# Performance work log

Measured on AMD Instinct MI355X. Metric: run time of the kernel, lower is better.

The kernel has to match this reference:

```python
import jax, jax.numpy as jnp
import numpy as np

N = 50000
NEG_SLOPE_ATT = 0.2    # PyG GATConv attention leaky_relu slope
NEG_SLOPE_ACT = 0.01   # torch F.leaky_relu default slope


def leaky(x, s):
    return jnp.where(x >= 0, x, s * x)


def gat_conv(x, src, dst, W, att_src, att_dst, bias):
    """PyG GATConv (concat=True, dropout off, self-loops already in src/dst).
    x: [N, F_in]; W: [F_in, H*C]; att_src/att_dst: [H, C]; bias: [H*C]."""
    H, C = att_src.shape
    h = (x @ W).reshape(N, H, C)                       # [N, H, C]
    a_src = (h * att_src[None]).sum(-1)                # [N, H]
    a_dst = (h * att_dst[None]).sum(-1)                # [N, H]
    e = leaky(a_src[src] + a_dst[dst], NEG_SLOPE_ATT)  # [E, H]
    # numerically-stable softmax over incoming edges of each dst node
    m = jax.ops.segment_max(e, dst, num_segments=N)    # [N, H]
    ex = jnp.exp(e - m[dst])
    Z = jax.ops.segment_sum(ex, dst, num_segments=N)   # [N, H]
    alpha = ex / (Z[dst] + 1e-16)                      # [E, H]
    msg = h[src] * alpha[:, :, None]                   # [E, H, C]
    out = jax.ops.segment_sum(msg, dst, num_segments=N)
    return out.reshape(N, H * C) + bias[None, :]


def setup_inputs() -> dict:
    key = jax.random.key(0)
    ks = jax.random.split(key, 12)
    E = 800000
    in_c, hid, heads, out_c = 256, 32, 4, 128
    hc = hid * heads  # 128
    x = jax.random.normal(ks[0], (N, in_c), dtype=jnp.float32)
    edge_index = jax.random.randint(ks[1], (2, E), 0, N, dtype=jnp.int64)
    s1 = 1.0 / np.sqrt(in_c)
    s2 = 1.0 / np.sqrt(hc)
    return {
        "x": x,
        "edge_index": edge_index,
        "W1": jax.random.normal(ks[2], (in_c, heads * hid), dtype=jnp.float32) * s1,
        "att_src1": jax.random.normal(ks[3], (heads, hid), dtype=jnp.float32) * s2,
        "att_dst1": jax.random.normal(ks[4], (heads, hid), dtype=jnp.float32) * s2,
        "b1": jnp.zeros((hc,), dtype=jnp.float32),
        "W2": jax.random.normal(ks[5], (hc, out_c), dtype=jnp.float32) * s2,
        "att_src2": jax.random.normal(ks[6], (1, out_c), dtype=jnp.float32) * s2,
        "att_dst2": jax.random.normal(ks[7], (1, out_c), dtype=jnp.float32) * s2,
        "b2": jnp.zeros((out_c,), dtype=jnp.float32),
    }


def reference(x, edge_index, W1, att_src1, att_dst1, b1, W2, att_src2, att_dst2, b2):
    # add self loops (PyG GATConv default add_self_loops=True)
    loops = jnp.arange(N, dtype=edge_index.dtype)
    src = jnp.concatenate([edge_index[0], loops])
    dst = jnp.concatenate([edge_index[1], loops])
    h = leaky(gat_conv(x, src, dst, W1, att_src1, att_dst1, b1), NEG_SLOPE_ACT)
    out = leaky(gat_conv(h, src, dst, W2, att_src2, att_dst2, b2), NEG_SLOPE_ACT)
    return out
```

## Files before the change

kernel.cpp:

```cpp
#include <hip/hip_runtime.h>
#include <hip/hip_fp16.h>

#define SLOPE_ATT 0.2f
#define SLOPE_ACT 0.01f

#define NB_CSR 128
#define CHUNK 8192

typedef _Float16 hf8 __attribute__((ext_vector_type(8)));
typedef float f32x4 __attribute__((ext_vector_type(4)));

template<int K, int H, bool A_FP32>
__device__ __forceinline__
void gemm_mfma_body(int gbid, int tid,
                    const void* __restrict__ Av, const _Float16* __restrict__ BT,
                    const float* __restrict__ att_s, const float* __restrict__ att_d,
                    _Float16* __restrict__ hout, float* __restrict__ a_src,
                    float* __restrict__ a_dst, int M)
{
  const int lane = tid & 63;
  const int wid  = tid >> 6;
  const int li   = lane & 15;
  const int lk   = lane >> 4;
  const int rowbase = gbid * 128 + wid * 32;

  const float*    Af = (const float*)Av;
  const _Float16* Ah = (const _Float16*)Av;

  f32x4 acc[2][8];
#pragma unroll
  for (int i = 0; i < 2; ++i)
#pragma unroll
    for (int j = 0; j < 8; ++j) acc[i][j] = (f32x4){0.f, 0.f, 0.f, 0.f};

  const int r0 = min(rowbase + li,      M - 1);
  const int r1 = min(rowbase + 16 + li, M - 1);

#pragma unroll
  for (int ks = 0; ks < K / 32; ++ks) {
    const int kb = ks * 32 + lk * 8;
    hf8 a0, a1;
    if constexpr (A_FP32) {
      const float* p0 = &Af[(size_t)r0 * K + kb];
      const float* p1 = &Af[(size_t)r1 * K + kb];
      float4 x0a = *(const float4*)p0, x0b = *(const float4*)(p0 + 4);
      float4 x1a = *(const float4*)p1, x1b = *(const float4*)(p1 + 4);
      a0[0]=(_Float16)x0a.x; a0[1]=(_Float16)x0a.y; a0[2]=(_Float16)x0a.z; a0[3]=(_Float16)x0a.w;
      a0[4]=(_Float16)x0b.x; a0[5]=(_Float16)x0b.y; a0[6]=(_Float16)x0b.z; a0[7]=(_Float16)x0b.w;
      a1[0]=(_Float16)x1a.x; a1[1]=(_Float16)x1a.y; a1[2]=(_Float16)x1a.z; a1[3]=(_Float16)x1a.w;
      a1[4]=(_Float16)x1b.x; a1[5]=(_Float16)x1b.y; a1[6]=(_Float16)x1b.z; a1[7]=(_Float16)x1b.w;
    } else {
      a0 = *(const hf8*)&Ah[(size_t)r0 * K + kb];
      a1 = *(const hf8*)&Ah[(size_t)r1 * K + kb];
    }
#pragma unroll
    for (int cf = 0; cf < 8; ++cf) {
      hf8 b = *(const hf8*)&BT[(size_t)(cf * 16 + li) * K + kb];
      acc[0][cf] = __builtin_amdgcn_mfma_f32_16x16x32_f16(a0, b, acc[0][cf], 0, 0, 0);
      acc[1][cf] = __builtin_amdgcn_mfma_f32_16x16x32_f16(a1, b, acc[1][cf], 0, 0, 0);
    }
  }

  float sA[8], dA[8];
#pragma unroll
  for (int cf = 0; cf < 8; ++cf) {
    sA[cf] = att_s[cf * 16 + li];
    dA[cf] = att_d[cf * 16 + li];
  }

  const bool full = (rowbase + 32) <= M;
#pragma unroll
  for (int rf = 0; rf < 2; ++rf) {
    const int rb = rowbase + rf * 16 + lk * 4;
#pragma unroll
    for (int reg = 0; reg < 4; ++reg) {
      const int r = rb + reg;
      if (full || r < M) {
#pragma unroll
        for (int cf = 0; cf < 8; ++cf)
          hout[(size_t)r * 128 + cf * 16 + li] = (_Float16)acc[rf][cf][reg];
      }
    }
    if constexpr (H == 4) {
#pragma unroll
      for (int hh = 0; hh < 4; ++hh) {
#pragma unroll
        for (int reg = 0; reg < 4; ++reg) {
          float sp = acc[rf][2*hh][reg] * sA[2*hh] + acc[rf][2*hh+1][reg] * sA[2*hh+1];
          float dp = acc[rf][2*hh][reg] * dA[2*hh] + acc[rf][2*hh+1][reg] * dA[2*hh+1];
          sp += __shfl_xor(sp, 1); sp += __shfl_xor(sp, 2);
          sp += __shfl_xor(sp, 4); sp += __shfl_xor(sp, 8);
          dp += __shfl_xor(dp, 1); dp += __shfl_xor(dp, 2);
          dp += __shfl_xor(dp, 4); dp += __shfl_xor(dp, 8);
          const int r = rb + reg;
          if (li == 0 && r < M) {
            a_src[(size_t)r * 4 + hh] = sp;
            a_dst[(size_t)r * 4 + hh] = dp;
          }
        }
      }
    } else {
#pragma unroll
      for (int reg = 0; reg < 4; ++reg) {
        float sp = 0.f, dp = 0.f;
#pragma unroll
        for (int cf = 0; cf < 8; ++cf) {
          sp += acc[rf][cf][reg] * sA[cf];
          dp += acc[rf][cf][reg] * dA[cf];
        }
        sp += __shfl_xor(sp, 1); sp += __shfl_xor(sp, 2);
        sp += __shfl_xor(sp, 4); sp += __shfl_xor(sp, 8);
        dp += __shfl_xor(dp, 1); dp += __shfl_xor(dp, 2);
        dp += __shfl_xor(dp, 4); dp += __shfl_xor(dp, 8);
        const int r = rb + reg;
        if (li == 0 && r < M) { a_src[r] = sp; a_dst[r] = dp; }
      }
    }
  }
}

template<int K, int H, bool A_FP32>
__global__ __launch_bounds__(256)
void gemm_mfma_kernel(const void* __restrict__ Av, const _Float16* __restrict__ BT,
                      const float* __restrict__ att_s, const float* __restrict__ att_d,
                      _Float16* __restrict__ hout, float* __restrict__ a_src,
                      float* __restrict__ a_dst, int M)
{
  gemm_mfma_body<K, H, A_FP32>(blockIdx.x, threadIdx.x, Av, BT, att_s, att_d,
                               hout, a_src, a_dst, M);
}

__global__ __launch_bounds__(256)
void fused_pre_kernel(const int* __restrict__ ei, int E, int N,
                      unsigned short* __restrict__ cnt16mat,
                      unsigned short* __restrict__ rank16,
                      const float* __restrict__ W1, _Float16* __restrict__ W1T,
                      const float* __restrict__ W2, _Float16* __restrict__ W2T,
                      int ncount)
{
  __shared__ unsigned cnt[CHUNK];
  const int bid = blockIdx.x;
  if (bid < ncount) {
    const int b = bid % NB_CSR;
    const int c0 = (bid / NB_CSR) * CHUNK;
    const int clen = min(CHUNK, N - c0);
    const int EE = E + N;
    const int epb = (EE + NB_CSR - 1) / NB_CSR;
    const int lo = b * epb, hi = min(lo + epb, EE);

    for (int j = threadIdx.x; j < clen; j += 256) cnt[j] = 0;
    __syncthreads();
    for (int i = lo + threadIdx.x; i < hi; i += 256) {
      int d = (i < E) ? ei[E + i] : (i - E);
      int r = d - c0;
      if (r >= 0 && r < clen) {
        unsigned rank = atomicAdd(&cnt[r], 1u);
        rank16[i] = (unsigned short)rank;
      }
    }
    __syncthreads();
    for (int j = threadIdx.x; j < clen; j += 256)
      cnt16mat[(size_t)b * N + c0 + j] = (unsigned short)cnt[j];
  } else {
    int rem = bid - ncount;
    if (rem < 128) {
      int idx = rem * 256 + threadIdx.x;
      int k = idx >> 7, c = idx & 127;
      W1T[(size_t)c * 256 + k] = (_Float16)W1[idx];
    } else {
      int idx = (rem - 128) * 256 + threadIdx.x;
      int k = idx >> 7, c = idx & 127;
      W2T[(size_t)c * 128 + k] = (_Float16)W2[idx];
    }
  }
}

__global__ __launch_bounds__(256)
void colscan_kernel(unsigned short* __restrict__ cnt16mat,
                    unsigned* __restrict__ deg, unsigned* __restrict__ bsum, int N)
{
  __shared__ unsigned red[256];
  const int d2 = blockIdx.x * 256 + threadIdx.x;
  const int N2 = N >> 1;
  unsigned off0 = 0, off1 = 0;
  if (d2 < N2) {
    unsigned* pm = (unsigned*)cnt16mat;
#pragma unroll 8
    for (int b = 0; b < NB_CSR; ++b) {
      unsigned t = pm[(size_t)b * N2 + d2];
      pm[(size_t)b * N2 + d2] = off0 | (off1 << 16);
      off0 += t & 0xFFFFu;
      off1 += t >> 16;
    }
    deg[2 * d2]     = off0;
    deg[2 * d2 + 1] = off1;
  }
  red[threadIdx.x] = off0 + off1;
  __syncthreads();
  for (int o = 128; o; o >>= 1) {
    if (threadIdx.x < o) red[threadIdx.x] += red[threadIdx.x + o];
    __syncthreads();
  }
  if (threadIdx.x == 0) bsum[blockIdx.x] = red[0];
}

__global__ __launch_bounds__(256)
void rowstart_kernel(const unsigned* __restrict__ deg, const unsigned* __restrict__ bsum,
                     unsigned* __restrict__ row_start, int N, int nblk)
{
  __shared__ unsigned s[256];
  __shared__ unsigned boff_sh;
  const int t = threadIdx.x;
  unsigned v0 = (t < nblk) ? bsum[t] : 0u;
  s[t] = v0;
  __syncthreads();
  for (int off = 1; off < 256; off <<= 1) {
    unsigned v = (t >= off) ? s[t - off] : 0u;
    __syncthreads();
    s[t] += v;
    __syncthreads();
  }
  if (t == (int)blockIdx.x) boff_sh = s[t] - v0;
  __syncthreads();
  const unsigned boff = boff_sh;
  __syncthreads();
  const int i = blockIdx.x * 512 + t * 2;
  unsigned d0 = (i < N) ? deg[i] : 0u;
  unsigned d1 = (i + 1 < N) ? deg[i + 1] : 0u;
  s[t] = d0 + d1;
  __syncthreads();
  for (int off = 1; off < 256; off <<= 1) {
    unsigned v = (t >= off) ? s[t - off] : 0u;
    __syncthreads();
    s[t] += v;
    __syncthreads();
  }
  unsigned base = boff + s[t] - (d0 + d1);
  if (i < N)     row_start[i] = base;
  if (i + 1 < N) row_start[i + 1] = base + d0;
}

__global__ __launch_bounds__(256)
void fused_mid_kernel(const int* __restrict__ ei, int E, int N, int epb,
                      const unsigned short* __restrict__ cnt16mat,
                      const unsigned short* __restrict__ rank16,
                      const unsigned* __restrict__ row_start,
                      unsigned* __restrict__ csr_src,
                      const float* __restrict__ x, const _Float16* __restrict__ W1T,
                      const float* __restrict__ as1, const float* __restrict__ ad1,
                      _Float16* __restrict__ h, float* __restrict__ asv,
                      float* __restrict__ adv, int ggrid)
{
  const int bid = blockIdx.x;
  if (bid < ggrid) {
    gemm_mfma_body<256, 4, true>(bid, threadIdx.x, x, W1T, as1, ad1,
                                 h, asv, adv, N);
  } else {
    const int i = (bid - ggrid) * 256 + threadIdx.x;
    const int EE = E + N;
    if (i < EE) {
      int s, d;
      if (i < E) { s = ei[i]; d = ei[E + i]; } else { s = d = i - E; }
      const int b = i / epb;
      unsigned pos = row_start[d] + cnt16mat[(size_t)b * N + d] + rank16[i];
      csr_src[pos] = (unsigned)s;
    }
  }
}

template<int H, bool OUT_HALF>
__global__ __launch_bounds__(256)
void aggregate_kernel(const unsigned* __restrict__ row_start,
                      const unsigned* __restrict__ deg,
                      const unsigned* __restrict__ csr_src,
                      const __half* __restrict__ h,
                      const float* __restrict__ a_src,
                      const float* __restrict__ a_dst,
                      const float* __restrict__ bias,
                      void* __restrict__ outv, int N)
{
  const int lane = threadIdx.x & 63;
  const int wid  = threadIdx.x >> 6;
  const int l5   = lane & 15;
  const int n    = blockIdx.x * 16 + wid * 4 + (lane >> 4);
  const int nn   = min(n, N - 1);
  const int hd   = (H == 4) ? (l5 >> 2) : 0;

  const float adn = a_dst[(size_t)nn * H + hd];
  const unsigned beg = row_start[nn];
  const unsigned cnt = deg[nn];
  unsigned cmax = cnt;
  cmax = max(cmax, (unsigned)__shfl_xor((int)cmax, 16));
  cmax = max(cmax, (unsigned)__shfl_xor((int)cmax, 32));

  const float4* __restrict__ h4 = (const float4*)h;

  float Z = 0.f;
  float acc[8];
#pragma unroll
  for (int j = 0; j < 8; ++j) acc[j] = 0.f;

  unsigned i = 0;
  for (; i + 2 <= cmax; i += 2) {
    unsigned s0 = csr_src[beg + min(i,     cnt - 1)];
    unsigned s1 = csr_src[beg + min(i + 1, cnt - 1)];
    float e0 = a_src[(size_t)s0 * H + hd] + adn;
    float e1 = a_src[(size_t)s1 * H + hd] + adn;
    float4 v0 = h4[(size_t)s0 * 16 + l5];
    float4 v1 = h4[(size_t)s1 * 16 + l5];
    e0 = (e0 >= 0.f) ? e0 : SLOPE_ATT * e0;
    e1 = (e1 >= 0.f) ? e1 : SLOPE_ATT * e1;
    float w0 = (i     < cnt) ? __expf(e0) : 0.f;
    float w1 = (i + 1 < cnt) ? __expf(e1) : 0.f;
    Z += w0 + w1;
    const __half2* p0 = (const __half2*)&v0;
    const __half2* p1 = (const __half2*)&v1;
#pragma unroll
    for (int j = 0; j < 4; ++j) {
      float2 f0 = __half22float2(p0[j]);
      float2 f1 = __half22float2(p1[j]);
      acc[2*j]   += w0 * f0.x + w1 * f1.x;
      acc[2*j+1] += w0 * f0.y + w1 * f1.y;
    }
  }
  if (i < cmax) {
    unsigned s0 = csr_src[beg + min(i, cnt - 1)];
    float e0 = a_src[(size_t)s0 * H + hd] + adn;
    float4 v0 = h4[(size_t)s0 * 16 + l5];
    e0 = (e0 >= 0.f) ? e0 : SLOPE_ATT * e0;
    float w0 = (i < cnt) ? __expf(e0) : 0.f;
    Z += w0;
    const __half2* p0 = (const __half2*)&v0;
#pragma unroll
    for (int j = 0; j < 4; ++j) {
      float2 f0 = __half22float2(p0[j]);
      acc[2*j]   += w0 * f0.x;
      acc[2*j+1] += w0 * f0.y;
    }
  }

  const float inv = 1.f / (Z + 1e-16f);
  float4 b0 = ((const float4*)bias)[l5 * 2];
  float4 b1 = ((const float4*)bias)[l5 * 2 + 1];
  float o[8];
  o[0] = acc[0] * inv + b0.x;  o[1] = acc[1] * inv + b0.y;
  o[2] = acc[2] * inv + b0.z;  o[3] = acc[3] * inv + b0.w;
  o[4] = acc[4] * inv + b1.x;  o[5] = acc[5] * inv + b1.y;
  o[6] = acc[6] * inv + b1.z;  o[7] = acc[7] * inv + b1.w;
#pragma unroll
  for (int j = 0; j < 8; ++j) o[j] = (o[j] >= 0.f) ? o[j] : SLOPE_ACT * o[j];

  if (n < N) {
    if constexpr (OUT_HALF) {
      union { __half2 q[4]; float4 f; } u;
      u.q[0] = __floats2half2_rn(o[0], o[1]);
      u.q[1] = __floats2half2_rn(o[2], o[3]);
      u.q[2] = __floats2half2_rn(o[4], o[5]);
      u.q[3] = __floats2half2_rn(o[6], o[7]);
      ((float4*)outv)[(size_t)n * 16 + l5] = u.f;
    } else {
      ((float4*)outv)[(size_t)n * 32 + l5 * 2]     = make_float4(o[0], o[1], o[2], o[3]);
      ((float4*)outv)[(size_t)n * 32 + l5 * 2 + 1] = make_float4(o[4], o[5], o[6], o[7]);
    }
  }
}

extern "C" void kernel_launch(void* const* d_in, const int* in_sizes, int n_in,
                              void* d_out, int out_size, void* d_ws, size_t ws_size,
                              hipStream_t stream)
{
  const float* x   = (const float*)d_in[0];
  const int*   ei  = (const int*)d_in[1];
  const float* W1  = (const float*)d_in[2];
  const float* as1 = (const float*)d_in[3];
  const float* ad1 = (const float*)d_in[4];
  const float* b1  = (const float*)d_in[5];
  const float* W2  = (const float*)d_in[6];
  const float* as2 = (const float*)d_in[7];
  const float* ad2 = (const float*)d_in[8];
  const float* b2  = (const float*)d_in[9];
  float* out = (float*)d_out;

  const int N  = in_sizes[0] / 256;
  const int E  = in_sizes[1] / 2;
  const int EE = E + N;
  const int NCH  = (N + CHUNK - 1) / CHUNK;
  const int nblk = (N + 511) / 512;
  const int NSC  = NB_CSR * NCH;
  const int epb  = (EE + NB_CSR - 1) / NB_CSR;

  float* ws = (float*)d_ws;
  size_t o = 0;
  _Float16* h    = (_Float16*)(ws + o); o += (size_t)N * 64;
  _Float16* act1 = (_Float16*)(ws + o); o += (size_t)N * 64;
  float* asv = ws + o; o += (size_t)N * 4;
  float* adv = ws + o; o += (size_t)N * 4;
  _Float16* W1T = (_Float16*)(ws + o); o += 128 * 256 / 2;
  _Float16* W2T = (_Float16*)(ws + o); o += 128 * 128 / 2;
  unsigned* deg       = (unsigned*)(ws + o); o += (size_t)N;
  unsigned* row_start = (unsigned*)(ws + o); o += (size_t)N;
  unsigned* bsum      = (unsigned*)(ws + o); o += 256;
  unsigned* csr_src   = (unsigned*)(ws + o); o += (size_t)EE;
  unsigned short* cnt16mat = (unsigned short*)(ws + o); o += (size_t)NB_CSR * N / 2;
  unsigned short* rank16   = (unsigned short*)(ws + o); o += (size_t)(EE + 1) / 2;

  const int ngrid = (N + 15) / 16;
  const int ggrid = (N + 127) / 128;
  const int sgrid = (EE + 255) / 256;

  fused_pre_kernel<<<NSC + 128 + 64, 256, 0, stream>>>(
      ei, E, N, cnt16mat, rank16, W1, W1T, W2, W2T, NSC);
  colscan_kernel<<<nblk, 256, 0, stream>>>(cnt16mat, deg, bsum, N);
  rowstart_kernel<<<nblk, 256, 0, stream>>>(deg, bsum, row_start, N, nblk);
  fused_mid_kernel<<<ggrid + sgrid, 256, 0, stream>>>(
      ei, E, N, epb, cnt16mat, rank16, row_start, csr_src,
      x, W1T, as1, ad1, h, asv, adv, ggrid);
  aggregate_kernel<4, true><<<ngrid, 256, 0, stream>>>(
      row_start, deg, csr_src, (const __half*)h, asv, adv, b1, act1, N);
  gemm_mfma_kernel<128, 1, false><<<ggrid, 256, 0, stream>>>(
      act1, W2T, as2, ad2, h, asv, adv, N);
  aggregate_kernel<1, false><<<ngrid, 256, 0, stream>>>(
      row_start, deg, csr_src, (const __half*)h, asv, adv, b2, out, N);
}
```

Baseline: 175.5 us.

## Fuse layer-1 aggregation with layer-2 GEMM and attention dots via LDS

The layer-1 aggregate kernel now writes each 16-node activation tile into shared memory and runs the layer-2 128x128 projection in the same block with MFMA. It also computes the layer-2 attention dot products using LDS atomics. This removes the act1 round trip through global memory and one kernel launch. In exchange the aggregation kernel gains LDS use, two block barriers and per-block W2T loads from global/L2, and uses small 16-row GEMM tiles that reuse weights less than the old 128-row GEMM did.

```diff
diff --git a/kernel.cpp b/kernel.cpp
--- a/kernel.cpp
+++ b/kernel.cpp
@@ -119,17 +119,6 @@
   }
 }
 
-template<int K, int H, bool A_FP32>
-__global__ __launch_bounds__(256)
-void gemm_mfma_kernel(const void* __restrict__ Av, const _Float16* __restrict__ BT,
-                      const float* __restrict__ att_s, const float* __restrict__ att_d,
-                      _Float16* __restrict__ hout, float* __restrict__ a_src,
-                      float* __restrict__ a_dst, int M)
-{
-  gemm_mfma_body<K, H, A_FP32>(blockIdx.x, threadIdx.x, Av, BT, att_s, att_d,
-                               hout, a_src, a_dst, M);
-}
-
 __global__ __launch_bounds__(256)
 void fused_pre_kernel(const int* __restrict__ ei, int E, int N,
                       unsigned short* __restrict__ cnt16mat,
@@ -268,25 +257,32 @@
   }
 }
 
-template<int H, bool OUT_HALF>
 __global__ __launch_bounds__(256)
-void aggregate_kernel(const unsigned* __restrict__ row_start,
-                      const unsigned* __restrict__ deg,
-                      const unsigned* __restrict__ csr_src,
-                      const __half* __restrict__ h,
-                      const float* __restrict__ a_src,
-                      const float* __restrict__ a_dst,
-                      const float* __restrict__ bias,
-                      void* __restrict__ outv, int N)
-{
+void agg1_gemm2_kernel(const unsigned* __restrict__ row_start,
+                       const unsigned* __restrict__ deg,
+                       const unsigned* __restrict__ csr_src,
+                       const __half* __restrict__ h,
+                       const float* __restrict__ a_src,
+                       const float* __restrict__ a_dst,
+                       const float* __restrict__ bias,
+                       const _Float16* __restrict__ W2T,
+                       const float* __restrict__ as2, const float* __restrict__ ad2,
+                       _Float16* __restrict__ h2,
+                       float* __restrict__ asv2, float* __restrict__ adv2, int N)
+{
+  __shared__ _Float16 actS[16][136];
+  __shared__ float sdots[2][16];
+
   const int lane = threadIdx.x & 63;
   const int wid  = threadIdx.x >> 6;
   const int l5   = lane & 15;
-  const int n    = blockIdx.x * 16 + wid * 4 + (lane >> 4);
+  const int nl   = wid * 4 + (lane >> 4);
+  const int nb   = blockIdx.x * 16;
+  const int n    = nb + nl;
   const int nn   = min(n, N - 1);
-  const int hd   = (H == 4) ? (l5 >> 2) : 0;
-
-  const float adn = a_dst[(size_t)nn * H + hd];
+  const int hd   = l5 >> 2;
+
+  const float adn = a_dst[(size_t)nn * 4 + hd];
   const unsigned beg = row_start[nn];
   const unsigned cnt = deg[nn];
   unsigned cmax = cnt;
@@ -304,8 +300,8 @@
   for (; i + 2 <= cmax; i += 2) {
     unsigned s0 = csr_src[beg + min(i,     cnt - 1)];
     unsigned s1 = csr_src[beg + min(i + 1, cnt - 1)];
-    float e0 = a_src[(size_t)s0 * H + hd] + adn;
-    float e1 = a_src[(size_t)s1 * H + hd] + adn;
+    float e0 = a_src[(size_t)s0 * 4 + hd] + adn;
+    float e1 = a_src[(size_t)s1 * 4 + hd] + adn;
     float4 v0 = h4[(size_t)s0 * 16 + l5];
     float4 v1 = h4[(size_t)s1 * 16 + l5];
     e0 = (e0 >= 0.f) ? e0 : SLOPE_ATT * e0;
@@ -325,7 +321,7 @@
   }
   if (i < cmax) {
     unsigned s0 = csr_src[beg + min(i, cnt - 1)];
-    float e0 = a_src[(size_t)s0 * H + hd] + adn;
+    float e0 = a_src[(size_t)s0 * 4 + hd] + adn;
     float4 v0 = h4[(size_t)s0 * 16 + l5];
     e0 = (e0 >= 0.f) ? e0 : SLOPE_ATT * e0;
     float w0 = (i < cnt) ? __expf(e0) : 0.f;
@@ -350,18 +346,135 @@
 #pragma unroll
   for (int j = 0; j < 8; ++j) o[j] = (o[j] >= 0.f) ? o[j] : SLOPE_ACT * o[j];
 
+#pragma unroll
+  for (int j = 0; j < 8; ++j) actS[nl][l5 * 8 + j] = (_Float16)o[j];
+  if (threadIdx.x < 32) sdots[threadIdx.x >> 4][threadIdx.x & 15] = 0.f;
+  __syncthreads();
+
+  const int li = l5;
+  const int lk = lane >> 4;
+#pragma unroll
+  for (int t = 0; t < 2; ++t) {
+    const int c0 = wid * 32 + t * 16;
+    f32x4 a2 = (f32x4){0.f, 0.f, 0.f, 0.f};
+#pragma unroll
+    for (int ks = 0; ks < 4; ++ks) {
+      hf8 af = *(const hf8*)&actS[li][ks * 32 + lk * 8];
+      hf8 bf = *(const hf8*)&W2T[(size_t)(c0 + li) * 128 + ks * 32 + lk * 8];
+      a2 = __builtin_amdgcn_mfma_f32_16x16x32_f16(af, bf, a2, 0, 0, 0);
+    }
+    const float asc = as2[c0 + li];
+    const float adc = ad2[c0 + li];
+#pragma unroll
+    for (int reg = 0; reg < 4; ++reg) {
+      const int r = lk * 4 + reg;
+      float hv = a2[reg];
+      if (nb + r < N) h2[(size_t)(nb + r) * 128 + c0 + li] = (_Float16)hv;
+      float sp = hv * asc;
+      float dp = hv * adc;
+      sp += __shfl_xor(sp, 1); sp += __shfl_xor(sp, 2);
+      sp += __shfl_xor(sp, 4); sp += __shfl_xor(sp, 8);
+      dp += __shfl_xor(dp, 1); dp += __shfl_xor(dp, 2);
+      dp += __shfl_xor(dp, 4); dp += __shfl_xor(dp, 8);
+      if (li == 0) {
+        atomicAdd(&sdots[0][r], sp);
+        atomicAdd(&sdots[1][r], dp);
+      }
+    }
+  }
+  __syncthreads();
+  if (threadIdx.x < 16) {
+    const int r = threadIdx.x;
+    if (nb + r < N) {
+      asv2[nb + r] = sdots[0][r];
+      adv2[nb + r] = sdots[1][r];
+    }
+  }
+}
+
+__global__ __launch_bounds__(256)
+void aggregate2_kernel(const unsigned* __restrict__ row_start,
+                       const unsigned* __restrict__ deg,
+                       const unsigned* __restrict__ csr_src,
+                       const __half* __restrict__ h,
+                       const float* __restrict__ a_src,
+                       const float* __restrict__ a_dst,
+                       const float* __restrict__ bias,
+                       float* __restrict__ out, int N)
+{
+  const int lane = threadIdx.x & 63;
+  const int wid  = threadIdx.x >> 6;
+  const int l5   = lane & 15;
+  const int n    = blockIdx.x * 16 + wid * 4 + (lane >> 4);
+  const int nn   = min(n, N - 1);
+
+  const float adn = a_dst[nn];
+  const unsigned beg = row_start[nn];
+  const unsigned cnt = deg[nn];
+  unsigned cmax = cnt;
+  cmax = max(cmax, (unsigned)__shfl_xor((int)cmax, 16));
+  cmax = max(cmax, (unsigned)__shfl_xor((int)cmax, 32));
+
+  const float4* __restrict__ h4 = (const float4*)h;
+
+  float Z = 0.f;
+  float acc[8];
+#pragma unroll
+  for (int j = 0; j < 8; ++j) acc[j] = 0.f;
+
+  unsigned i = 0;
+  for (; i + 2 <= cmax; i += 2) {
+    unsigned s0 = csr_src[beg + min(i,     cnt - 1)];
+    unsigned s1 = csr_src[beg + min(i + 1, cnt - 1)];
+    float e0 = a_src[s0] + adn;
+    float e1 = a_src[s1] + adn;
+    float4 v0 = h4[(size_t)s0 * 16 + l5];
+    float4 v1 = h4[(size_t)s1 * 16 + l5];
+    e0 = (e0 >= 0.f) ? e0 : SLOPE_ATT * e0;
+    e1 = (e1 >= 0.f) ? e1 : SLOPE_ATT * e1;
+    float w0 = (i     < cnt) ? __expf(e0) : 0.f;
+    float w1 = (i + 1 < cnt) ? __expf(e1) : 0.f;
+    Z += w0 + w1;
+    const __half2* p0 = (const __half2*)&v0;
+    const __half2* p1 = (const __half2*)&v1;
+#pragma unroll
+    for (int j = 0; j < 4; ++j) {
+      float2 f0 = __half22float2(p0[j]);
+      float2 f1 = __half22float2(p1[j]);
+      acc[2*j]   += w0 * f0.x + w1 * f1.x;
+      acc[2*j+1] += w0 * f0.y + w1 * f1.y;
+    }
+  }
+  if (i < cmax) {
+    unsigned s0 = csr_src[beg + min(i, cnt - 1)];
+    float e0 = a_src[s0] + adn;
+    float4 v0 = h4[(size_t)s0 * 16 + l5];
+    e0 = (e0 >= 0.f) ? e0 : SLOPE_ATT * e0;
+    float w0 = (i < cnt) ? __expf(e0) : 0.f;
+    Z += w0;
+    const __half2* p0 = (const __half2*)&v0;
+#pragma unroll
+    for (int j = 0; j < 4; ++j) {
+      float2 f0 = __half22float2(p0[j]);
+      acc[2*j]   += w0 * f0.x;
+      acc[2*j+1] += w0 * f0.y;
+    }
+  }
+
+  const float inv = 1.f / (Z + 1e-16f);
+  float4 b0 = ((const float4*)bias)[l5 * 2];
+  float4 b1 = ((const float4*)bias)[l5 * 2 + 1];
+  float o[8];
+  o[0] = acc[0] * inv + b0.x;  o[1] = acc[1] * inv + b0.y;
+  o[2] = acc[2] * inv + b0.z;  o[3] = acc[3] * inv + b0.w;
+  o[4] = acc[4] * inv + b1.x;  o[5] = acc[5] * inv + b1.y;
+  o[6] = acc[6] * inv + b1.z;  o[7] = acc[7] * inv + b1.w;
+#pragma unroll
+  for (int j = 0; j < 8; ++j) o[j] = (o[j] >= 0.f) ? o[j] : SLOPE_ACT * o[j];
+
   if (n < N) {
-    if constexpr (OUT_HALF) {
-      union { __half2 q[4]; float4 f; } u;
-      u.q[0] = __floats2half2_rn(o[0], o[1]);
-      u.q[1] = __floats2half2_rn(o[2], o[3]);
-      u.q[2] = __floats2half2_rn(o[4], o[5]);
-      u.q[3] = __floats2half2_rn(o[6], o[7]);
-      ((float4*)outv)[(size_t)n * 16 + l5] = u.f;
-    } else {
-      ((float4*)outv)[(size_t)n * 32 + l5 * 2]     = make_float4(o[0], o[1], o[2], o[3]);
-      ((float4*)outv)[(size_t)n * 32 + l5 * 2 + 1] = make_float4(o[4], o[5], o[6], o[7]);
-    }
+    ((float4*)out)[(size_t)n * 32 + l5 * 2]     = make_float4(o[0], o[1], o[2], o[3]);
+    ((float4*)out)[(size_t)n * 32 + l5 * 2 + 1] = make_float4(o[4], o[5], o[6], o[7]);
   }
 }
 
@@ -392,9 +505,11 @@
   float* ws = (float*)d_ws;
   size_t o = 0;
   _Float16* h    = (_Float16*)(ws + o); o += (size_t)N * 64;
-  _Float16* act1 = (_Float16*)(ws + o); o += (size_t)N * 64;
-  float* asv = ws + o; o += (size_t)N * 4;
-  float* adv = ws + o; o += (size_t)N * 4;
+  _Float16* h2   = (_Float16*)(ws + o); o += (size_t)N * 64;
+  float* asv  = ws + o; o += (size_t)N * 4;
+  float* adv  = ws + o; o += (size_t)N * 4;
+  float* asv2 = ws + o; o += (size_t)N;
+  float* adv2 = ws + o; o += (size_t)N;
   _Float16* W1T = (_Float16*)(ws + o); o += 128 * 256 / 2;
   _Float16* W2T = (_Float16*)(ws + o); o += 128 * 128 / 2;
   unsigned* deg       = (unsigned*)(ws + o); o += (size_t)N;
@@ -415,10 +530,9 @@
   fused_mid_kernel<<<ggrid + sgrid, 256, 0, stream>>>(
       ei, E, N, epb, cnt16mat, rank16, row_start, csr_src,
       x, W1T, as1, ad1, h, asv, adv, ggrid);
-  aggregate_kernel<4, true><<<ngrid, 256, 0, stream>>>(
-      row_start, deg, csr_src, (const __half*)h, asv, adv, b1, act1, N);
-  gemm_mfma_kernel<128, 1, false><<<ggrid, 256, 0, stream>>>(
-      act1, W2T, as2, ad2, h, asv, adv, N);
-  aggregate_kernel<1, false><<<ngrid, 256, 0, stream>>>(
-      row_start, deg, csr_src, (const __half*)h, asv, adv, b2, out, N);
-}
+  agg1_gemm2_kernel<<<ngrid, 256, 0, stream>>>(
+      row_start, deg, csr_src, (const __half*)h, asv, adv, b1,
+      W2T, as2, ad2, h2, asv2, adv2, N);
+  aggregate2_kernel<<<ngrid, 256, 0, stream>>>(
+      row_start, deg, csr_src, (const __half*)h2, asv2, adv2, b2, out, N);
+}
```

Result: faster. 170.0 us (-3.2%).
